# Performance work log

Hardware: AMD Instinct MI355X
Metric: run time of the kernel (lower is better)

Reference implementation:

```python
import jax, jax.numpy as jnp
import numpy as np

DT_RANK = 64
N_STATES = 16


def selective_scan(u, delta, A, B, C, D):
    # u,delta: [b,l,d]; A: [d,n]; B,C: [b,l,n]; D: [d]
    dA = jnp.einsum('bld,dn->bldn', delta, A)
    dB_u = jnp.einsum('bld,bld,bln->bldn', delta, u, B)
    # shifted exclusive suffix-sum: cum[t] = sum_{s=t+1}^{L-1} dA[s]
    dA_shift = jnp.concatenate([dA[:, 1:], jnp.zeros_like(dA[:, :1])], axis=1)
    dA_cumsum = jnp.exp(jnp.flip(jnp.cumsum(jnp.flip(dA_shift, axis=1), axis=1), axis=1))
    xs = jnp.cumsum(dB_u * dA_cumsum, axis=1) / (dA_cumsum + 1e-12)
    y = jnp.einsum('bldn,bln->bld', xs, C)
    return y + u * D


def setup_inputs() -> dict:
    key = jax.random.key(0)
    ks = jax.random.split(key, 6)
    b, l, d = 2, 1024, 1024
    dt_rank, n = DT_RANK, N_STATES
    x = jax.random.normal(ks[0], (b, l, d), dtype=jnp.float32)
    # Dense kernels with glorot-ish scale
    W_x = jax.random.normal(ks[1], (d, dt_rank + 2 * n), dtype=jnp.float32) * (1.0 / np.sqrt(d))
    W_dt = jax.random.normal(ks[2], (dt_rank, d), dtype=jnp.float32) * (1.0 / np.sqrt(dt_rank))
    b_dt = jnp.zeros((d,), dtype=jnp.float32)
    # A_log = log(repeat(1..n, d)) as in S6.__init__
    A_log = jnp.log(jnp.tile(jnp.arange(1, n + 1, dtype=jnp.float32)[None, :], (d, 1)))
    D = jnp.ones((d,), dtype=jnp.float32)
    W_out = jax.random.normal(ks[3], (d, d), dtype=jnp.float32) * (1.0 / np.sqrt(d))
    b_out = jnp.zeros((d,), dtype=jnp.float32)
    return {"x": x, "W_x": W_x, "W_dt": W_dt, "b_dt": b_dt,
            "A_log": A_log, "D": D, "W_out": W_out, "b_out": b_out}


def reference(x, W_x, W_dt, b_dt, A_log, D, W_out, b_out):
    n = A_log.shape[1]
    A = -jnp.exp(A_log)                     # [d,n]
    x_dbl = jnp.einsum('bld,de->ble', x, W_x)  # [b,l,dt_rank+2n]
    delta = x_dbl[..., :DT_RANK]
    B = x_dbl[..., DT_RANK:DT_RANK + n]
    C = x_dbl[..., DT_RANK + n:]
    delta = jax.nn.softplus(jnp.einsum('blr,rd->bld', delta, W_dt) + b_dt)
    y = selective_scan(x, delta, A, B, C, D)
    return jnp.einsum('bld,de->ble', y, W_out) + b_out
```

## Files before the change

kernel.cpp:

```cpp
#include <hip/hip_runtime.h>
#include <hip/hip_bf16.h>

#define LSEQ 1024
#define DMODEL 1024
#define NSTATE 16
#define DTRANK 64
#define ECOL 96
#define MTOT 2048

typedef short s16x8 __attribute__((ext_vector_type(8)));
typedef float f32x4 __attribute__((ext_vector_type(4)));
typedef unsigned int u32x4 __attribute__((ext_vector_type(4)));

#if __has_builtin(__builtin_amdgcn_exp2f)
#define EXP2F(x) __builtin_amdgcn_exp2f(x)
#else
#define EXP2F(x) exp2f(x)
#endif
#define LOG2E 1.4426950408889634

__device__ inline unsigned short f2bf(float f) {
    unsigned int u = __builtin_bit_cast(unsigned int, f);
    u += 0x7FFFu + ((u >> 16) & 1u);
    return (unsigned short)(u >> 16);
}
__device__ inline float bf2f(unsigned short h) {
    unsigned int u = ((unsigned int)h) << 16;
    return __builtin_bit_cast(float, u);
}
__device__ inline f32x4 bfq2f(ushort4 h) {
    f32x4 r;
    r[0] = bf2f(h.x); r[1] = bf2f(h.y); r[2] = bf2f(h.z); r[3] = bf2f(h.w);
    return r;
}

__device__ inline f32x4 shflup4(f32x4 v, int off) {
    f32x4 r;
    r[0] = __shfl_up(v[0], off, 64);
    r[1] = __shfl_up(v[1], off, 64);
    r[2] = __shfl_up(v[2], off, 64);
    r[3] = __shfl_up(v[3], off, 64);
    return r;
}

__global__ __launch_bounds__(256) void k_xdbl(const float* __restrict__ x,
                                              const float* __restrict__ Wx,
                                              const float* __restrict__ Wdt,
                                              const float* __restrict__ Wout,
                                              float* __restrict__ part,
                                              unsigned short* __restrict__ WdtTh,
                                              unsigned short* __restrict__ WdtTl,
                                              unsigned short* __restrict__ WbfT) {
    __shared__ alignas(16) char pool[32768];
    int bid = blockIdx.x;
    int tid = threadIdx.x;

    if (bid >= 256) {
        float (*t)[65] = (float (*)[65])pool;
        if (bid < 320) {
            int id3 = bid - 256;
            int d0 = (id3 & 31) * 32, r0 = (id3 >> 5) * 32;
            int tx = tid & 31, ty = tid >> 5;
#pragma unroll
            for (int j = 0; j < 32; j += 8)
                t[ty + j][tx] = Wdt[(size_t)(r0 + ty + j) * 1024 + d0 + tx];
            __syncthreads();
#pragma unroll
            for (int j = 0; j < 32; j += 8) {
                float v = t[tx][ty + j];
                unsigned short h = f2bf(v);
                WdtTh[(size_t)(d0 + ty + j) * 64 + r0 + tx] = h;
                WdtTl[(size_t)(d0 + ty + j) * 64 + r0 + tx] = f2bf(v - bf2f(h));
            }
        } else {
            int id4 = bid - 320;
            int e0 = (id4 & 15) * 64, k0 = (id4 >> 4) * 64;
            int tx = tid & 63, ty = tid >> 6;
#pragma unroll
            for (int j = 0; j < 64; j += 4)
                t[ty + j][tx] = Wout[(size_t)(k0 + ty + j) * 1024 + e0 + tx];
            __syncthreads();
#pragma unroll
            for (int j = 0; j < 64; j += 4)
                WbfT[(size_t)(e0 + ty + j) * 1024 + k0 + tx] = f2bf(t[tx][ty + j]);
        }
        return;
    }

    unsigned short* Ah = (unsigned short*)pool;
    unsigned short* Al = (unsigned short*)(pool + 4096);
    unsigned short* Bh = (unsigned short*)(pool + 8192);
    unsigned short* Bl = (unsigned short*)(pool + 20480);
    int bm = (bid >> 2) * 32;
    int slice = bid & 3;
    int lane = tid & 63, w = tid >> 6;
    int wm = w >> 1, wn = w & 1;
    int r = lane & 15, kb = lane >> 4;

    f32x4 acc[3];
#pragma unroll
    for (int nf = 0; nf < 3; ++nf) acc[nf] = (f32x4){0.f, 0.f, 0.f, 0.f};

#pragma unroll 1
    for (int kc = 0; kc < 4; ++kc) {
        int kbase = slice * 256 + kc * 64;
        __syncthreads();
        {
            int row = tid >> 3, cc = tid & 7;
            size_t src = (size_t)(bm + row) * 1024 + kbase + cc * 8;
            float4 v0 = *(const float4*)&x[src];
            float4 v1 = *(const float4*)&x[src + 4];
            float vv[8] = {v0.x, v0.y, v0.z, v0.w, v1.x, v1.y, v1.z, v1.w};
            s16x8 h, lo;
#pragma unroll
            for (int j = 0; j < 8; ++j) {
                unsigned short hb = f2bf(vv[j]);
                h[j] = (short)hb;
                lo[j] = (short)f2bf(vv[j] - bf2f(hb));
            }
            int dstB = row * 128 + ((cc * 16) ^ ((row & 7) << 4));
            *(s16x8*)((char*)Ah + dstB) = h;
            *(s16x8*)((char*)Al + dstB) = lo;
        }
#pragma unroll
        for (int it = 0; it < 3; ++it) {
            int item = it * 256 + tid;
            int e = item % 96;
            int cc = item / 96;
            s16x8 h, lo;
#pragma unroll
            for (int j = 0; j < 8; ++j) {
                float v = Wx[(size_t)(kbase + cc * 8 + j) * 96 + e];
                unsigned short hb = f2bf(v);
                h[j] = (short)hb;
                lo[j] = (short)f2bf(v - bf2f(hb));
            }
            int dstB = e * 128 + ((cc * 16) ^ ((e & 7) << 4));
            *(s16x8*)((char*)Bh + dstB) = h;
            *(s16x8*)((char*)Bl + dstB) = lo;
        }
        __syncthreads();
#pragma unroll
        for (int ks = 0; ks < 2; ++ks) {
            int sw = (ks * 64 + kb * 16) ^ ((r & 7) << 4);
            s16x8 a_h = *(const s16x8*)((char*)Ah + (wm * 16 + r) * 128 + sw);
            s16x8 a_l = *(const s16x8*)((char*)Al + (wm * 16 + r) * 128 + sw);
#pragma unroll
            for (int nf = 0; nf < 3; ++nf) {
                int brow = wn * 48 + nf * 16 + r;
                s16x8 b_h = *(const s16x8*)((char*)Bh + brow * 128 + sw);
                s16x8 b_l = *(const s16x8*)((char*)Bl + brow * 128 + sw);
                acc[nf] = __builtin_amdgcn_mfma_f32_16x16x32_bf16(a_h, b_h, acc[nf], 0, 0, 0);
                acc[nf] = __builtin_amdgcn_mfma_f32_16x16x32_bf16(a_h, b_l, acc[nf], 0, 0, 0);
                acc[nf] = __builtin_amdgcn_mfma_f32_16x16x32_bf16(a_l, b_h, acc[nf], 0, 0, 0);
            }
        }
    }
    float* pb = part + (size_t)slice * 2048 * 96;
#pragma unroll
    for (int nf = 0; nf < 3; ++nf)
#pragma unroll
        for (int j = 0; j < 4; ++j)
            pb[(size_t)(bm + wm * 16 + kb * 4 + j) * 96 + wn * 48 + nf * 16 + r] = acc[nf][j];
}

__global__ __launch_bounds__(256) void k_delta2(const float* __restrict__ part,
                                                const unsigned short* __restrict__ WdtTh,
                                                const unsigned short* __restrict__ WdtTl,
                                                const float* __restrict__ bdt,
                                                const float* __restrict__ x,
                                                float* __restrict__ deltaT,
                                                unsigned short* __restrict__ bpk,
                                                unsigned short* __restrict__ cpk,
                                                unsigned short* __restrict__ xTbf) {
    __shared__ alignas(16) char pool[34816];
    int bid = blockIdx.x;
    int tid = threadIdx.x;

    if (bid >= 256) {
        float (*t)[65] = (float (*)[65])pool;
        int id = bid - 256;
        int d0 = (id & 15) * 64, m0 = (id >> 4) * 64;
        int tx = tid & 63, ty = tid >> 6;
#pragma unroll
        for (int j = 0; j < 64; j += 4)
            t[ty + j][tx] = x[(size_t)(m0 + ty + j) * 1024 + d0 + tx];
        __syncthreads();
#pragma unroll
        for (int j = 0; j < 64; j += 4)
            xTbf[(size_t)(d0 + ty + j) * 2048 + m0 + tx] = f2bf(t[tx][ty + j]);
        return;
    }

    unsigned short* Ah = (unsigned short*)pool;
    unsigned short* Al = (unsigned short*)(pool + 16384);
    float (*slab)[32][68] = (float (*)[32][68])pool;
    int bxq = bid & 15, byq = bid >> 4;
    int bm = byq * 128;
    int bn = bxq * 64;
    int lane = tid & 63, w = tid >> 6;
    int wm = w >> 1, wn = w & 1;
    int r = lane & 15, kb = lane >> 4;

#pragma unroll
    for (int i = 0; i < 8; ++i) {
        int q = tid + i * 256;
        int row = q >> 4, c4 = q & 15;
        size_t off = (size_t)(bm + row) * 96 + c4 * 4;
        f32x4 v = *(const f32x4*)&part[off];
#pragma unroll
        for (int s = 1; s < 4; ++s) v += *(const f32x4*)&part[(size_t)s * 2048 * 96 + off];
        ushort4 h4, l4;
        h4.x = f2bf(v[0]); l4.x = f2bf(v[0] - bf2f(h4.x));
        h4.y = f2bf(v[1]); l4.y = f2bf(v[1] - bf2f(h4.y));
        h4.z = f2bf(v[2]); l4.z = f2bf(v[2] - bf2f(h4.z));
        h4.w = f2bf(v[3]); l4.w = f2bf(v[3] - bf2f(h4.w));
        int dstB = row * 128 + ((c4 * 8) ^ ((row & 7) << 4));
        *(ushort4*)((char*)Ah + dstB) = h4;
        *(ushort4*)((char*)Al + dstB) = l4;
    }
    if (bxq == 0) {
#pragma unroll
        for (int i = 0; i < 4; ++i) {
            int q = tid + i * 256;
            int row = q >> 3, c4 = q & 7;
            size_t off = (size_t)(bm + row) * 96 + 64 + c4 * 4;
            f32x4 v = *(const f32x4*)&part[off];
#pragma unroll
            for (int s = 1; s < 4; ++s) v += *(const f32x4*)&part[(size_t)s * 2048 * 96 + off];
            ushort4 o;
            o.x = f2bf(v[0]); o.y = f2bf(v[1]); o.z = f2bf(v[2]); o.w = f2bf(v[3]);
            if (c4 < 4) *(ushort4*)&bpk[(size_t)(bm + row) * 16 + c4 * 4] = o;
            else        *(ushort4*)&cpk[(size_t)(bm + row) * 16 + (c4 - 4) * 4] = o;
        }
    }
    __syncthreads();

    f32x4 acc[4][2];
#pragma unroll
    for (int mf = 0; mf < 4; ++mf)
#pragma unroll
        for (int nf = 0; nf < 2; ++nf) acc[mf][nf] = (f32x4){0.f, 0.f, 0.f, 0.f};

#pragma unroll
    for (int ks = 0; ks < 2; ++ks) {
        int sw = (ks * 64 + kb * 16) ^ ((r & 7) << 4);
        s16x8 Afh[4], Afl[4], Bh[2], Bl[2];
#pragma unroll
        for (int mf = 0; mf < 4; ++mf) {
            int arow = wm * 64 + mf * 16 + r;
            Afh[mf] = *(const s16x8*)((char*)Ah + arow * 128 + sw);
            Afl[mf] = *(const s16x8*)((char*)Al + arow * 128 + sw);
        }
#pragma unroll
        for (int nf = 0; nf < 2; ++nf) {
            size_t b = (size_t)(bn + wn * 32 + nf * 16 + r) * 64 + ks * 32 + kb * 8;
            Bh[nf] = *(const s16x8*)&WdtTh[b];
            Bl[nf] = *(const s16x8*)&WdtTl[b];
        }
#pragma unroll
        for (int mf = 0; mf < 4; ++mf)
#pragma unroll
            for (int nf = 0; nf < 2; ++nf) {
                acc[mf][nf] = __builtin_amdgcn_mfma_f32_16x16x32_bf16(Afh[mf], Bh[nf], acc[mf][nf], 0, 0, 0);
                acc[mf][nf] = __builtin_amdgcn_mfma_f32_16x16x32_bf16(Afh[mf], Bl[nf], acc[mf][nf], 0, 0, 0);
                acc[mf][nf] = __builtin_amdgcn_mfma_f32_16x16x32_bf16(Afl[mf], Bh[nf], acc[mf][nf], 0, 0, 0);
            }
    }
    __syncthreads();

#pragma unroll
    for (int nf = 0; nf < 2; ++nf) {
        float bb = bdt[bn + wn * 32 + nf * 16 + r];
#pragma unroll
        for (int mf = 0; mf < 4; ++mf)
#pragma unroll
            for (int j = 0; j < 4; ++j) {
                float z = acc[mf][nf][j] + bb;
                float sp = fmaxf(z, 0.f) + log1pf(expf(-fabsf(z)));
                slab[w][nf * 16 + r][mf * 16 + kb * 4 + j] = sp;
            }
    }
#pragma unroll
    for (int i = 0; i < 8; ++i) {
        int idx = i * 64 + lane;
        int dl = idx >> 4, mq = (idx & 15) * 4;
        f32x4 v = *(const f32x4*)&slab[w][dl][mq];
        *(f32x4*)&deltaT[(size_t)(bn + wn * 32 + dl) * MTOT + bm + wm * 64 + mq] = v;
    }
}

__global__ __launch_bounds__(256) void k_scan3(const float* __restrict__ deltaT,
                                               const unsigned short* __restrict__ xTbf,
                                               const unsigned short* __restrict__ bpk,
                                               const unsigned short* __restrict__ cpk,
                                               const float* __restrict__ Alog,
                                               const float* __restrict__ Dp,
                                               unsigned short* __restrict__ yTbf) {
    __shared__ double csum[64];
    __shared__ double Rbef[64];
    __shared__ float TcL[64 * 20];
    __shared__ float syp[64 * 17];

    int tid = threadIdx.x;
    int c = tid >> 2, l = tid & 3;
    int w = tid >> 6, lane = tid & 63;
    int d = blockIdx.x & 1023, b = blockIdx.x >> 10;
    int m0 = b * 1024;

    const f32x4* dp = (const f32x4*)(deltaT + (size_t)d * MTOT + m0 + c * 16);
    const unsigned short* up = xTbf + (size_t)d * MTOT + m0 + c * 16;
    const unsigned short* Bp = bpk + (size_t)(m0 + c * 16) * 16 + l * 4;
    const unsigned short* Cp = cpk + (size_t)(m0 + c * 16) * 16 + l * 4;

    double dsum = 0.0;
#pragma unroll
    for (int i = 0; i < 4; ++i) {
        f32x4 v = dp[i];
        dsum += (double)v[0] + (double)v[1] + (double)v[2] + (double)v[3];
    }
    if (l == 0) csum[c] = dsum;
    __syncthreads();
    if (tid < 64) {
        double v = csum[tid];
#pragma unroll
        for (int off = 1; off < 64; off <<= 1) {
            double t = __shfl_down(v, off, 64);
            if (tid + off < 64) v += t;
        }
        Rbef[tid] = v;
    }
    __syncthreads();

    float Af2[4], Sb2[4];
    double Rb = Rbef[c];
#pragma unroll
    for (int j = 0; j < 4; ++j) {
        float Af = -__expf(Alog[d * NSTATE + 4 * l + j]);
        double A2 = (double)Af * LOG2E;
        Af2[j] = (float)A2;
        Sb2[j] = (float)(A2 * Rb);
    }
    float Dv = Dp[d];

    float P = 0.f;
    f32x4 Tn = {0.f, 0.f, 0.f, 0.f};
#pragma unroll 1
    for (int t4 = 0; t4 < 4; ++t4) {
        f32x4 rdv = dp[t4];
        ushort4 uv = *(const ushort4*)(up + t4 * 4);
        float ru[4] = {bf2f(uv.x), bf2f(uv.y), bf2f(uv.z), bf2f(uv.w)};
        f32x4 Bq[4];
#pragma unroll
        for (int k = 0; k < 4; ++k)
            Bq[k] = bfq2f(*(const ushort4*)(Bp + (size_t)(t4 * 4 + k) * 16));
#pragma unroll
        for (int k = 0; k < 4; ++k) {
            float dlt = rdv[k];
            P += dlt;
            float du = dlt * ru[k];
#pragma unroll
            for (int j = 0; j < 4; ++j) {
                float e = EXP2F(fmaf(-Af2[j], P, Sb2[j]));
                Tn[j] = fmaf(du * Bq[k][j], e, Tn[j]);
            }
        }
    }
    *(f32x4*)&TcL[c * 20 + 4 * l] = Tn;
    __syncthreads();

    {
        f32x4 v = *(const f32x4*)&TcL[lane * 20 + 4 * w];
#pragma unroll
        for (int off = 1; off < 64; off <<= 1) {
            f32x4 t = shflup4(v, off);
            if (lane >= off) v += t;
        }
        f32x4 ex = shflup4(v, 1);
        if (lane == 0) ex = (f32x4){0.f, 0.f, 0.f, 0.f};
        *(f32x4*)&TcL[lane * 20 + 4 * w] = ex;
    }
    __syncthreads();
    f32x4 num = *(const f32x4*)&TcL[c * 20 + 4 * l];

    P = 0.f;
#pragma unroll 1
    for (int t4 = 0; t4 < 4; ++t4) {
        f32x4 rdv = dp[t4];
        ushort4 uv = *(const ushort4*)(up + t4 * 4);
        float ru[4] = {bf2f(uv.x), bf2f(uv.y), bf2f(uv.z), bf2f(uv.w)};
        f32x4 Bq[4], Cq[4];
#pragma unroll
        for (int k = 0; k < 4; ++k) {
            Bq[k] = bfq2f(*(const ushort4*)(Bp + (size_t)(t4 * 4 + k) * 16));
            Cq[k] = bfq2f(*(const ushort4*)(Cp + (size_t)(t4 * 4 + k) * 16));
        }
#pragma unroll
        for (int k = 0; k < 4; ++k) {
            float dlt = rdv[k];
            P += dlt;
            float du = dlt * ru[k];
            float psum = 0.f;
#pragma unroll
            for (int j = 0; j < 4; ++j) {
                float e = EXP2F(fmaf(-Af2[j], P, Sb2[j]));
                num[j] = fmaf(du * Bq[k][j], e, num[j]);
                float rr = __builtin_amdgcn_rcpf(e + 1e-12f);
                psum = fmaf(num[j] * rr, Cq[k][j], psum);
            }
            psum += __shfl_xor(psum, 1);
            psum += __shfl_xor(psum, 2);
            if (l == 0) syp[c * 17 + t4 * 4 + k] = fmaf(ru[k], Dv, psum);
        }
    }
    __syncthreads();
    {
        int cc = tid >> 2, oo = (tid & 3) * 4;
        const float* sp = &syp[cc * 17 + oo];
        ushort4 o;
        o.x = f2bf(sp[0]);
        o.y = f2bf(sp[1]);
        o.z = f2bf(sp[2]);
        o.w = f2bf(sp[3]);
        *reinterpret_cast<ushort4*>(&yTbf[(size_t)d * MTOT + m0 + tid * 4]) = o;
    }
}

__global__ __launch_bounds__(256) void k_gemm(const unsigned short* __restrict__ yT,
                                              const unsigned short* __restrict__ B,
                                              const float* __restrict__ bias,
                                              float* __restrict__ out) {
    __shared__ unsigned int P[2][32 * 68];
    __shared__ unsigned short Bs[2][64 * 64];
    const int GN = 1024, GK = 1024;
    int bm = blockIdx.y * 64;
    int bn = blockIdx.x * 64;
    int tid = threadIdx.x;
    int lane = tid & 63;
    int w = tid >> 6;
    int wm = w >> 1, wn = w & 1;
    int r = lane & 15, kb = lane >> 4;

    f32x4 acc[2][2];
#pragma unroll
    for (int mf = 0; mf < 2; ++mf)
#pragma unroll
        for (int nf = 0; nf < 2; ++nf) acc[mf][nf] = (f32x4){0.f, 0.f, 0.f, 0.f};

    ushort4 rya[2], ryb[2];
    s16x8 rbv[2];
    auto stage_load = [&](int k0) {
#pragma unroll
        for (int i = 0; i < 2; ++i) {
            int slot = tid + i * 256;
            int p = slot >> 4, mq = (slot & 15) * 4;
            rya[i] = *(const ushort4*)&yT[(size_t)(k0 + 2 * p) * MTOT + bm + mq];
            ryb[i] = *(const ushort4*)&yT[(size_t)(k0 + 2 * p + 1) * MTOT + bm + mq];
            rbv[i] = *(const s16x8*)&B[(size_t)(bn + (slot >> 3)) * GK + k0 + (slot & 7) * 8];
        }
    };

    stage_load(0);
    int cur = 0;
    for (int k0 = 0; k0 < GK; k0 += 64) {
#pragma unroll
        for (int i = 0; i < 2; ++i) {
            int slot = tid + i * 256;
            int p = slot >> 4, mq = (slot & 15) * 4;
            u32x4 pk;
            pk[0] = (unsigned int)rya[i].x | ((unsigned int)ryb[i].x << 16);
            pk[1] = (unsigned int)rya[i].y | ((unsigned int)ryb[i].y << 16);
            pk[2] = (unsigned int)rya[i].z | ((unsigned int)ryb[i].z << 16);
            pk[3] = (unsigned int)rya[i].w | ((unsigned int)ryb[i].w << 16);
            *(u32x4*)&P[cur][p * 68 + mq] = pk;
            int row = slot >> 3;
            int dstB = row * 128 + (((slot & 7) * 16) ^ ((row & 7) << 4));
            *(s16x8*)((char*)&Bs[cur][0] + dstB) = rbv[i];
        }
        __syncthreads();
        if (k0 + 64 < GK) stage_load(k0 + 64);
#pragma unroll
        for (int ks = 0; ks < 2; ++ks) {
            int sw = (ks * 64 + kb * 16) ^ ((r & 7) << 4);
            s16x8 af[2], bfr[2];
#pragma unroll
            for (int mf = 0; mf < 2; ++mf) {
                int base = (ks * 16 + kb * 4) * 68 + wm * 32 + mf * 16 + r;
                u32x4 av;
                av[0] = P[cur][base];
                av[1] = P[cur][base + 68];
                av[2] = P[cur][base + 136];
                av[3] = P[cur][base + 204];
                af[mf] = __builtin_bit_cast(s16x8, av);
            }
#pragma unroll
            for (int nf = 0; nf < 2; ++nf)
                bfr[nf] = *(const s16x8*)((char*)&Bs[cur][0] + (wn * 32 + nf * 16 + r) * 128 + sw);
#pragma unroll
            for (int mf = 0; mf < 2; ++mf)
#pragma unroll
                for (int nf = 0; nf < 2; ++nf)
                    acc[mf][nf] = __builtin_amdgcn_mfma_f32_16x16x32_bf16(af[mf], bfr[nf], acc[mf][nf], 0, 0, 0);
        }
        cur ^= 1;
    }
#pragma unroll
    for (int nf = 0; nf < 2; ++nf) {
        float bb = bias[bn + wn * 32 + nf * 16 + r];
#pragma unroll
        for (int mf = 0; mf < 2; ++mf)
#pragma unroll
            for (int j = 0; j < 4; ++j)
                out[(size_t)(bm + wm * 32 + mf * 16 + kb * 4 + j) * GN + bn + wn * 32 + nf * 16 + r] =
                    acc[mf][nf][j] + bb;
    }
}

extern "C" void kernel_launch(void* const* d_in, const int* in_sizes, int n_in,
                              void* d_out, int out_size, void* d_ws, size_t ws_size,
                              hipStream_t stream) {
    const float* x    = (const float*)d_in[0];
    const float* Wx   = (const float*)d_in[1];
    const float* Wdt  = (const float*)d_in[2];
    const float* bdt  = (const float*)d_in[3];
    const float* Alog = (const float*)d_in[4];
    const float* Dp   = (const float*)d_in[5];
    const float* Wout = (const float*)d_in[6];
    const float* bout = (const float*)d_in[7];
    float* out = (float*)d_out;

    float* deltaT = (float*)d_ws;
    float* part   = deltaT + 1024 * 2048;
    unsigned short* bpk   = (unsigned short*)(part + 4 * 2048 * 96);
    unsigned short* cpk   = bpk + 2048 * 16;
    unsigned short* xTbf  = cpk + 2048 * 16;
    unsigned short* WdtTh = xTbf + 1024 * 2048;
    unsigned short* WdtTl = WdtTh + 1024 * 64;
    unsigned short* yTbf  = WdtTl + 1024 * 64;
    unsigned short* WbfT  = yTbf + 1024 * 2048;

    k_xdbl<<<576, 256, 0, stream>>>(x, Wx, Wdt, Wout, part, WdtTh, WdtTl, WbfT);
    k_delta2<<<768, 256, 0, stream>>>(part, WdtTh, WdtTl, bdt, x, deltaT, bpk, cpk, xTbf);
    k_scan3<<<2048, 256, 0, stream>>>(deltaT, xTbf, bpk, cpk, Alog, Dp, yTbf);
    k_gemm<<<dim3(16, 32), 256, 0, stream>>>(yTbf, WbfT, bout, out);
}
```

Measured before the change: 64.65 us.

## Move x transpose into first kernel and halve output GEMM M-tile

```diff
diff --git a/kernel.cpp b/kernel.cpp
--- a/kernel.cpp
+++ b/kernel.cpp
@@ -50,7 +50,8 @@
                                               float* __restrict__ part,
                                               unsigned short* __restrict__ WdtTh,
                                               unsigned short* __restrict__ WdtTl,
-                                              unsigned short* __restrict__ WbfT) {
+                                              unsigned short* __restrict__ WbfT,
+                                              unsigned short* __restrict__ xTbf) {
     __shared__ alignas(16) char pool[32768];
     int bid = blockIdx.x;
     int tid = threadIdx.x;
@@ -72,7 +73,7 @@
                 WdtTh[(size_t)(d0 + ty + j) * 64 + r0 + tx] = h;
                 WdtTl[(size_t)(d0 + ty + j) * 64 + r0 + tx] = f2bf(v - bf2f(h));
             }
-        } else {
+        } else if (bid < 576) {
             int id4 = bid - 320;
             int e0 = (id4 & 15) * 64, k0 = (id4 >> 4) * 64;
             int tx = tid & 63, ty = tid >> 6;
@@ -83,6 +84,17 @@
 #pragma unroll
             for (int j = 0; j < 64; j += 4)
                 WbfT[(size_t)(e0 + ty + j) * 1024 + k0 + tx] = f2bf(t[tx][ty + j]);
+        } else {
+            int id = bid - 576;
+            int d0 = (id & 15) * 64, m0 = (id >> 4) * 64;
+            int tx = tid & 63, ty = tid >> 6;
+#pragma unroll
+            for (int j = 0; j < 64; j += 4)
+                t[ty + j][tx] = x[(size_t)(m0 + ty + j) * 1024 + d0 + tx];
+            __syncthreads();
+#pragma unroll
+            for (int j = 0; j < 64; j += 4)
+                xTbf[(size_t)(d0 + ty + j) * 2048 + m0 + tx] = f2bf(t[tx][ty + j]);
         }
         return;
     }
@@ -168,29 +180,12 @@
                                                 const unsigned short* __restrict__ WdtTh,
                                                 const unsigned short* __restrict__ WdtTl,
                                                 const float* __restrict__ bdt,
-                                                const float* __restrict__ x,
                                                 float* __restrict__ deltaT,
                                                 unsigned short* __restrict__ bpk,
-                                                unsigned short* __restrict__ cpk,
-                                                unsigned short* __restrict__ xTbf) {
+                                                unsigned short* __restrict__ cpk) {
     __shared__ alignas(16) char pool[34816];
     int bid = blockIdx.x;
     int tid = threadIdx.x;
-
-    if (bid >= 256) {
-        float (*t)[65] = (float (*)[65])pool;
-        int id = bid - 256;
-        int d0 = (id & 15) * 64, m0 = (id >> 4) * 64;
-        int tx = tid & 63, ty = tid >> 6;
-#pragma unroll
-        for (int j = 0; j < 64; j += 4)
-            t[ty + j][tx] = x[(size_t)(m0 + ty + j) * 1024 + d0 + tx];
-        __syncthreads();
-#pragma unroll
-        for (int j = 0; j < 64; j += 4)
-            xTbf[(size_t)(d0 + ty + j) * 2048 + m0 + tx] = f2bf(t[tx][ty + j]);
-        return;
-    }
 
     unsigned short* Ah = (unsigned short*)pool;
     unsigned short* Al = (unsigned short*)(pool + 16384);
@@ -430,10 +425,10 @@
                                               const unsigned short* __restrict__ B,
                                               const float* __restrict__ bias,
                                               float* __restrict__ out) {
-    __shared__ unsigned int P[2][32 * 68];
+    __shared__ unsigned int P[2][32 * 36];
     __shared__ unsigned short Bs[2][64 * 64];
     const int GN = 1024, GK = 1024;
-    int bm = blockIdx.y * 64;
+    int bm = blockIdx.y * 32;
     int bn = blockIdx.x * 64;
     int tid = threadIdx.x;
     int lane = tid & 63;
@@ -441,21 +436,19 @@
     int wm = w >> 1, wn = w & 1;
     int r = lane & 15, kb = lane >> 4;
 
-    f32x4 acc[2][2];
-#pragma unroll
-    for (int mf = 0; mf < 2; ++mf)
-#pragma unroll
-        for (int nf = 0; nf < 2; ++nf) acc[mf][nf] = (f32x4){0.f, 0.f, 0.f, 0.f};
-
-    ushort4 rya[2], ryb[2];
+    f32x4 acc[2];
+    acc[0] = (f32x4){0.f, 0.f, 0.f, 0.f};
+    acc[1] = (f32x4){0.f, 0.f, 0.f, 0.f};
+
+    ushort4 rya, ryb;
     s16x8 rbv[2];
     auto stage_load = [&](int k0) {
+        int p = tid >> 3, mq = (tid & 7) * 4;
+        rya = *(const ushort4*)&yT[(size_t)(k0 + 2 * p) * MTOT + bm + mq];
+        ryb = *(const ushort4*)&yT[(size_t)(k0 + 2 * p + 1) * MTOT + bm + mq];
 #pragma unroll
         for (int i = 0; i < 2; ++i) {
             int slot = tid + i * 256;
-            int p = slot >> 4, mq = (slot & 15) * 4;
-            rya[i] = *(const ushort4*)&yT[(size_t)(k0 + 2 * p) * MTOT + bm + mq];
-            ryb[i] = *(const ushort4*)&yT[(size_t)(k0 + 2 * p + 1) * MTOT + bm + mq];
             rbv[i] = *(const s16x8*)&B[(size_t)(bn + (slot >> 3)) * GK + k0 + (slot & 7) * 8];
         }
     };
@@ -463,44 +456,39 @@
     stage_load(0);
     int cur = 0;
     for (int k0 = 0; k0 < GK; k0 += 64) {
-#pragma unroll
-        for (int i = 0; i < 2; ++i) {
-            int slot = tid + i * 256;
-            int p = slot >> 4, mq = (slot & 15) * 4;
+        {
+            int p = tid >> 3, mq = (tid & 7) * 4;
             u32x4 pk;
-            pk[0] = (unsigned int)rya[i].x | ((unsigned int)ryb[i].x << 16);
-            pk[1] = (unsigned int)rya[i].y | ((unsigned int)ryb[i].y << 16);
-            pk[2] = (unsigned int)rya[i].z | ((unsigned int)ryb[i].z << 16);
-            pk[3] = (unsigned int)rya[i].w | ((unsigned int)ryb[i].w << 16);
-            *(u32x4*)&P[cur][p * 68 + mq] = pk;
-            int row = slot >> 3;
-            int dstB = row * 128 + (((slot & 7) * 16) ^ ((row & 7) << 4));
-            *(s16x8*)((char*)&Bs[cur][0] + dstB) = rbv[i];
+            pk[0] = (unsigned int)rya.x | ((unsigned int)ryb.x << 16);
+            pk[1] = (unsigned int)rya.y | ((unsigned int)ryb.y << 16);
+            pk[2] = (unsigned int)rya.z | ((unsigned int)ryb.z << 16);
+            pk[3] = (unsigned int)rya.w | ((unsigned int)ryb.w << 16);
+            *(u32x4*)&P[cur][p * 36 + mq] = pk;
+#pragma unroll
+            for (int i = 0; i < 2; ++i) {
+                int slot = tid + i * 256;
+                int row = slot >> 3;
+                int dstB = row * 128 + (((slot & 7) * 16) ^ ((row & 7) << 4));
+                *(s16x8*)((char*)&Bs[cur][0] + dstB) = rbv[i];
+            }
         }
         __syncthreads();
         if (k0 + 64 < GK) stage_load(k0 + 64);
 #pragma unroll
         for (int ks = 0; ks < 2; ++ks) {
             int sw = (ks * 64 + kb * 16) ^ ((r & 7) << 4);
-            s16x8 af[2], bfr[2];
-#pragma unroll
-            for (int mf = 0; mf < 2; ++mf) {
-                int base = (ks * 16 + kb * 4) * 68 + wm * 32 + mf * 16 + r;
-                u32x4 av;
-                av[0] = P[cur][base];
-                av[1] = P[cur][base + 68];
-                av[2] = P[cur][base + 136];
-                av[3] = P[cur][base + 204];
-                af[mf] = __builtin_bit_cast(s16x8, av);
-            }
-#pragma unroll
-            for (int nf = 0; nf < 2; ++nf)
-                bfr[nf] = *(const s16x8*)((char*)&Bs[cur][0] + (wn * 32 + nf * 16 + r) * 128 + sw);
-#pragma unroll
-            for (int mf = 0; mf < 2; ++mf)
-#pragma unroll
-                for (int nf = 0; nf < 2; ++nf)
-                    acc[mf][nf] = __builtin_amdgcn_mfma_f32_16x16x32_bf16(af[mf], bfr[nf], acc[mf][nf], 0, 0, 0);
+            int base = (ks * 16 + kb * 4) * 36 + wm * 16 + r;
+            u32x4 av;
+            av[0] = P[cur][base];
+            av[1] = P[cur][base + 36];
+            av[2] = P[cur][base + 72];
+            av[3] = P[cur][base + 108];
+            s16x8 af = __builtin_bit_cast(s16x8, av);
+#pragma unroll
+            for (int nf = 0; nf < 2; ++nf) {
+                s16x8 bfr = *(const s16x8*)((char*)&Bs[cur][0] + (wn * 32 + nf * 16 + r) * 128 + sw);
+                acc[nf] = __builtin_amdgcn_mfma_f32_16x16x32_bf16(af, bfr, acc[nf], 0, 0, 0);
+            }
         }
         cur ^= 1;
     }
@@ -508,11 +496,9 @@
     for (int nf = 0; nf < 2; ++nf) {
         float bb = bias[bn + wn * 32 + nf * 16 + r];
 #pragma unroll
-        for (int mf = 0; mf < 2; ++mf)
-#pragma unroll
-            for (int j = 0; j < 4; ++j)
-                out[(size_t)(bm + wm * 32 + mf * 16 + kb * 4 + j) * GN + bn + wn * 32 + nf * 16 + r] =
-                    acc[mf][nf][j] + bb;
+        for (int j = 0; j < 4; ++j)
+            out[(size_t)(bm + wm * 16 + kb * 4 + j) * GN + bn + wn * 32 + nf * 16 + r] =
+                acc[nf][j] + bb;
     }
 }
 
@@ -539,8 +525,8 @@
     unsigned short* yTbf  = WdtTl + 1024 * 64;
     unsigned short* WbfT  = yTbf + 1024 * 2048;
 
-    k_xdbl<<<576, 256, 0, stream>>>(x, Wx, Wdt, Wout, part, WdtTh, WdtTl, WbfT);
-    k_delta2<<<768, 256, 0, stream>>>(part, WdtTh, WdtTl, bdt, x, deltaT, bpk, cpk, xTbf);
+    k_xdbl<<<1088, 256, 0, stream>>>(x, Wx, Wdt, Wout, part, WdtTh, WdtTl, WbfT, xTbf);
+    k_delta2<<<256, 256, 0, stream>>>(part, WdtTh, WdtTl, bdt, deltaT, bpk, cpk);
     k_scan3<<<2048, 256, 0, stream>>>(deltaT, xTbf, bpk, cpk, Alog, Dp, yTbf);
-    k_gemm<<<dim3(16, 32), 256, 0, stream>>>(yTbf, WbfT, bout, out);
-}
+    k_gemm<<<dim3(16, 64), 256, 0, stream>>>(yTbf, WbfT, bout, out);
+}
```

New measurement: 68.02 us. +5.2%, slower.
